# Optimization experiments

Hardware: AMD Instinct MI355X
Metric: run time of the kernel (lower is better)

The kernel has to match this reference:

```python
import jax, jax.numpy as jnp
import numpy as np

DIM = 512
HEADS = 8
HD = DIM // HEADS
HIDDEN = 4 * DIM
EPS = 1e-5


def layernorm(x, g, b):
    mu = jnp.mean(x, axis=-1, keepdims=True)
    var = jnp.mean(jnp.square(x - mu), axis=-1, keepdims=True)
    return (x - mu) * jax.lax.rsqrt(var + EPS) * g + b


def setup_inputs() -> dict:
    key = jax.random.key(0)
    ks = jax.random.split(key, 10)
    B, P, N, C = 16, 4, 256, DIM
    s = 1.0 / np.sqrt(C)
    sh = 1.0 / np.sqrt(HIDDEN)
    return {
        "x": jax.random.normal(ks[0], (B, P, N, C), jnp.float32),
        "ln1_g": jnp.ones((C,), jnp.float32),
        "ln1_b": jnp.zeros((C,), jnp.float32),
        "w_qkv": jax.random.uniform(ks[1], (3 * C, C), jnp.float32, -s, s),
        "w_proj": jax.random.uniform(ks[2], (C, C), jnp.float32, -s, s),
        "b_proj": jax.random.uniform(ks[3], (C,), jnp.float32, -s, s),
        "ln2_g": jnp.ones((C,), jnp.float32),
        "ln2_b": jnp.zeros((C,), jnp.float32),
        "w1": jax.random.uniform(ks[4], (HIDDEN, C), jnp.float32, -s, s),
        "b1": jax.random.uniform(ks[5], (HIDDEN,), jnp.float32, -s, s),
        "w2": jax.random.uniform(ks[6], (C, HIDDEN), jnp.float32, -sh, sh),
        "b2": jax.random.uniform(ks[7], (C,), jnp.float32, -sh, sh),
    }


def reference(x, ln1_g, ln1_b, w_qkv, w_proj, b_proj, ln2_g, ln2_b, w1, b1, w2, b2):
    B, P, N, C = x.shape
    # --- attention branch (batched over B, P, heads; same math as the unrolled loops) ---
    h = layernorm(x, ln1_g, ln1_b)
    qkv = jnp.einsum('bpnc,dc->bpnd', h, w_qkv)            # [B,P,N,3C]
    qkv = qkv.reshape(B, P, N, 3, HEADS, HD)
    q, k, v = qkv[..., 0, :, :], qkv[..., 1, :, :], qkv[..., 2, :, :]  # [B,P,N,H,hd]
    scale = HD ** -0.5
    attn = jnp.einsum('bpnhd,bpmhd->bphnm', q * scale, k)  # [B,P,H,N,N]
    attn = jax.nn.softmax(attn, axis=-1)
    o = jnp.einsum('bphnm,bpmhd->bpnhd', attn, v).reshape(B, P, N, C)
    o = jnp.einsum('bpnc,dc->bpnd', o, w_proj) + b_proj
    x = x + o
    # --- MLP branch ---
    h = layernorm(x, ln2_g, ln2_b)
    h = jax.nn.gelu(jnp.einsum('bpnc,hc->bpnh', h, w1) + b1, approximate=False)
    h = jnp.einsum('bpnh,ch->bpnc', h, w2) + b2
    return x + h
```

## Files before the change

kernel.cpp:

```cpp
#include <hip/hip_runtime.h>

typedef __attribute__((ext_vector_type(8))) short short8;
typedef __attribute__((ext_vector_type(4))) float f32x4;

__device__ __forceinline__ float bf2f(unsigned short u) {
    return __uint_as_float(((unsigned)u) << 16);
}
__device__ __forceinline__ unsigned short f2bf(float f) {
    unsigned u = __float_as_uint(f);
    u += 0x7fffu + ((u >> 16) & 1u);
    return (unsigned short)(u >> 16);
}
__device__ __forceinline__ void load_lds16(const void* g, void* l) {
    __builtin_amdgcn_global_load_lds(
        (const __attribute__((address_space(1))) void*)g,
        (__attribute__((address_space(3))) void*)l, 16, 0, 0);
}
__device__ __forceinline__ bool is_bf16(const unsigned* dt) {
    return *dt == 0x3F803F80u;
}
__device__ __forceinline__ float gelu_fast(float t) {
    float u = t * (0.7978845608f + 0.0356774081f * t * t);
    float e = __expf(-2.0f * fabsf(u));
    float th = (1.0f - e) / (1.0f + e);
    th = copysignf(th, u);
    return 0.5f * t * (1.0f + th);
}

__global__ __launch_bounds__(512) void cast_all(
    const void* s_wqkv, const void* s_wproj, const void* s_w1, const void* s_w2,
    const void* v0, const void* v1, const void* v2, const void* v3,
    const void* v4, const void* v5, const void* v6,
    unsigned short* d_wqkv, unsigned short* d_wproj, unsigned short* d_w1,
    unsigned short* d_w2, unsigned short* par, const unsigned* dt)
{
    bool isbf = is_bf16(dt);
    int b = blockIdx.x, tid = threadIdx.x;
    if (b < 768) {
        const void* src; unsigned short* dst; int off;
        if (b < 192)      { src = s_wqkv;  dst = d_wqkv;  off = b * 4096; }
        else if (b < 256) { src = s_wproj; dst = d_wproj; off = (b - 192) * 4096; }
        else if (b < 512) { src = s_w1;    dst = d_w1;    off = (b - 256) * 4096; }
        else              { src = s_w2;    dst = d_w2;    off = (b - 512) * 4096; }
        int i = off + tid * 8;
        if (isbf) {
            *(short8*)(dst + i) = *(const short8*)((const unsigned short*)src + i);
        } else {
            const float* s = (const float*)src + i;
            short8 o;
            #pragma unroll
            for (int j = 0; j < 8; ++j) o[j] = (short)f2bf(s[j]);
            *(short8*)(dst + i) = o;
        }
    } else {
        const void* srcs[7]  = {v0, v1, v2, v3, v4, v5, v6};
        const int   sizes[7] = {512, 512, 512, 512, 512, 2048, 512};
        const int   offs[7]  = {0, 512, 1024, 1536, 2048, 2560, 4608};
        int j = b - 768;
        const void* s = srcs[j];
        unsigned short* d = par + offs[j];
        for (int i = tid; i < sizes[j]; i += 512)
            d[i] = isbf ? ((const unsigned short*)s)[i] : f2bf(((const float*)s)[i]);
    }
}

__global__ __launch_bounds__(256) void ln_kernel(
    const void* __restrict__ xin, size_t row0,
    const unsigned* __restrict__ dt, int force_f32,
    const unsigned short* __restrict__ g, const unsigned short* __restrict__ b,
    unsigned short* __restrict__ y)
{
    int w = threadIdx.x >> 6, lane = threadIdx.x & 63;
    size_t lr = (size_t)blockIdx.x * 4 + w;
    size_t gr = row0 + lr;
    bool isf32 = force_f32 || !is_bf16(dt);
    float v[8];
    if (isf32) {
        const float* xr = (const float*)xin + (gr << 9) + (lane << 3);
        #pragma unroll
        for (int j = 0; j < 8; ++j) v[j] = xr[j];
    } else {
        short8 raw = *(const short8*)((const unsigned short*)xin + (gr << 9) + (lane << 3));
        #pragma unroll
        for (int j = 0; j < 8; ++j) v[j] = bf2f((unsigned short)raw[j]);
    }
    float sum = 0.f, sq = 0.f;
    #pragma unroll
    for (int j = 0; j < 8; ++j) { sum += v[j]; sq += v[j] * v[j]; }
    #pragma unroll
    for (int off = 32; off > 0; off >>= 1) {
        sum += __shfl_xor(sum, off);
        sq  += __shfl_xor(sq, off);
    }
    float mu  = sum * (1.0f / 512.0f);
    float var = sq * (1.0f / 512.0f) - mu * mu;
    float rs  = rsqrtf(var + 1e-5f);
    short8 gr8 = *(const short8*)(g + (lane << 3));
    short8 br8 = *(const short8*)(b + (lane << 3));
    short8 outv;
    #pragma unroll
    for (int j = 0; j < 8; ++j) {
        float o = (v[j] - mu) * rs * bf2f((unsigned short)gr8[j]) + bf2f((unsigned short)br8[j]);
        outv[j] = (short)f2bf(o);
    }
    *(short8*)(y + (lr << 9) + (lane << 3)) = outv;
}

__global__ __launch_bounds__(256, 2) void gemm5(
    const unsigned short* __restrict__ A, const unsigned short* __restrict__ W,
    const unsigned short* __restrict__ bias,
    const void* __restrict__ resid, size_t rrow0,
    void* __restrict__ out, size_t orow0,
    int NBY, int N, int K, int mode, const unsigned* __restrict__ dt)
{
    constexpr int BM = 256, BN = 128;
    constexpr int MI = 8;
    constexpr int BUFB = (BM + BN) * 64;
    __shared__ char lds[BM * BN * 2];

    int tid = threadIdx.x;
    int w = tid >> 6, lane = tid & 63;
    int l15 = lane & 15, g = lane >> 4;

    int L = blockIdx.x;
    int bx, by;
    if ((NBY & 7) == 0) {
        int nby8 = NBY >> 3;
        int xcd = L & 7, i = L >> 3;
        by = xcd * nby8 + (i % nby8);
        bx = i / nby8;
    } else {
        by = L % NBY;
        bx = L / NBY;
    }
    int m0 = by << 8, n0 = bx << 7;
    int wm = (w >> 1) << 7;
    int wn = (w & 1) << 6;

    int srow_t = ((tid >> 3) << 1) | (tid & 1);
    int u_t = ((tid >> 1) & 3) ^ ((tid >> 3) & 3);
    const unsigned short* gA[4];
    const unsigned short* gB[2];
    #pragma unroll
    for (int j = 0; j < 4; ++j)
        gA[j] = A + (size_t)(m0 + j * 64 + srow_t) * K + u_t * 8;
    #pragma unroll
    for (int j = 0; j < 2; ++j)
        gB[j] = W + (size_t)(n0 + j * 64 + srow_t) * K + u_t * 8;
    int lslot = tid * 16;

    int off = (l15 >> 1) * 128 + ((g ^ ((l15 >> 1) & 3)) << 5) + ((l15 & 1) << 4);

    f32x4 acc[MI][4];
    #pragma unroll
    for (int i = 0; i < MI; ++i)
        #pragma unroll
        for (int j = 0; j < 4; ++j) acc[i][j] = (f32x4){0.f, 0.f, 0.f, 0.f};

    #pragma unroll
    for (int j = 0; j < 4; ++j)
        load_lds16(gA[j], &lds[j * 4096 + lslot]);
    #pragma unroll
    for (int j = 0; j < 2; ++j)
        load_lds16(gB[j], &lds[16384 + j * 4096 + lslot]);

    int p = 0;
    for (int k = 0; k < K; k += 32) {
        __syncthreads();
        if (k + 32 < K) {
            int kn = k + 32;
            char* nb = &lds[(p ^ 1) * BUFB];
            #pragma unroll
            for (int j = 0; j < 4; ++j)
                load_lds16(gA[j] + kn, nb + j * 4096 + lslot);
            #pragma unroll
            for (int j = 0; j < 2; ++j)
                load_lds16(gB[j] + kn, nb + 16384 + j * 4096 + lslot);
        }
        const char* bA = &lds[p * BUFB];
        const char* bB = bA + 16384;
        short8 af[MI], bfr[4];
        #pragma unroll
        for (int i = 0; i < MI; ++i)
            af[i] = *(const short8*)(bA + (wm + i * 16) * 64 + off);
        #pragma unroll
        for (int j = 0; j < 4; ++j)
            bfr[j] = *(const short8*)(bB + (wn + j * 16) * 64 + off);
        #pragma unroll
        for (int i = 0; i < MI; ++i)
            #pragma unroll
            for (int j = 0; j < 4; ++j)
                acc[i][j] = __builtin_amdgcn_mfma_f32_16x16x32_bf16(af[i], bfr[j], acc[i][j], 0, 0, 0);
        p ^= 1;
    }

    char* tb = (char*)lds;
    __syncthreads();
    #pragma unroll
    for (int j = 0; j < 4; ++j) {
        int colL = wn + j * 16 + l15;
        int ccb = colL >> 3, cb = (colL & 7) << 1;
        #pragma unroll
        for (int i = 0; i < MI; ++i) {
            #pragma unroll
            for (int r = 0; r < 4; ++r) {
                int row = wm + i * 16 + g * 4 + r;
                *(unsigned short*)(tb + row * 256 + ((ccb ^ (row & 15)) << 4) + cb)
                    = f2bf(acc[i][j][r]);
            }
        }
    }
    __syncthreads();

    int rL = tid >> 4;
    int lc = tid & 15;
    bool inbf = is_bf16(dt);
    int colg = n0 + lc * 8;
    float bv[8];
    if (bias) {
        short8 bb = *(const short8*)(bias + colg);
        #pragma unroll
        for (int t = 0; t < 8; ++t) bv[t] = bf2f((unsigned short)bb[t]);
    } else {
        #pragma unroll
        for (int t = 0; t < 8; ++t) bv[t] = 0.f;
    }

    for (int ps = 0; ps < 16; ++ps) {
        int row = ps * 16 + rL;
        int rowL = m0 + row;
        short8 vv = *(const short8*)(tb + row * 256 + ((lc ^ (row & 15)) << 4));
        float vals[8];
        #pragma unroll
        for (int t = 0; t < 8; ++t) vals[t] = bf2f((unsigned short)vv[t]) + bv[t];

        if (mode == 0) {
            *(short8*)((unsigned short*)out + (size_t)rowL * N + colg) = vv;
        } else if (mode == 2) {
            short8 ov;
            #pragma unroll
            for (int t = 0; t < 8; ++t) ov[t] = (short)f2bf(gelu_fast(vals[t]));
            *(short8*)((unsigned short*)out + (size_t)rowL * N + colg) = ov;
        } else if (mode == 1) {
            size_t rbase = (rrow0 + rowL) * (size_t)N + colg;
            float o8[8];
            if (inbf) {
                short8 rr = *(const short8*)((const unsigned short*)resid + rbase);
                #pragma unroll
                for (int t = 0; t < 8; ++t) o8[t] = bf2f((unsigned short)rr[t]) + vals[t];
            } else {
                f32x4 r0 = *(const f32x4*)((const float*)resid + rbase);
                f32x4 r1 = *(const f32x4*)((const float*)resid + rbase + 4);
                #pragma unroll
                for (int t = 0; t < 4; ++t) { o8[t] = r0[t] + vals[t]; o8[t + 4] = r1[t] + vals[t + 4]; }
            }
            float* ob = (float*)out + (size_t)rowL * N + colg;
            *(f32x4*)ob       = (f32x4){o8[0], o8[1], o8[2], o8[3]};
            *(f32x4*)(ob + 4) = (f32x4){o8[4], o8[5], o8[6], o8[7]};
        } else {
            size_t rbase = (size_t)rowL * N + colg;
            f32x4 r0 = *(const f32x4*)((const float*)resid + rbase);
            f32x4 r1 = *(const f32x4*)((const float*)resid + rbase + 4);
            float o8[8];
            #pragma unroll
            for (int t = 0; t < 4; ++t) { o8[t] = r0[t] + vals[t]; o8[t + 4] = r1[t] + vals[t + 4]; }
            size_t obase = (orow0 + rowL) * (size_t)N + colg;
            if (inbf) {
                short8 ov;
                #pragma unroll
                for (int t = 0; t < 8; ++t) ov[t] = (short)f2bf(o8[t]);
                *(short8*)((unsigned short*)out + obase) = ov;
            } else {
                float* ob = (float*)out + obase;
                *(f32x4*)ob       = (f32x4){o8[0], o8[1], o8[2], o8[3]};
                *(f32x4*)(ob + 4) = (f32x4){o8[4], o8[5], o8[6], o8[7]};
            }
        }
    }
}

__global__ __launch_bounds__(256) void attn_mfma(
    const unsigned short* __restrict__ qkv, unsigned short* __restrict__ o)
{
    __shared__ unsigned short Vt[64 * 256];
    __shared__ unsigned short Ps[4][16 * 256];
    int bp = blockIdx.x >> 3, h = blockIdx.x & 7;
    const unsigned short* base = qkv + (size_t)bp * 256 * 1536;
    int qo = h << 6, ko = 512 + (h << 6), vo = 1024 + (h << 6);
    int tid = threadIdx.x, w = tid >> 6, lane = tid & 63;
    int l15 = lane & 15, g = lane >> 4;

    {
        int d = tid & 63;
        for (int s = tid >> 6; s < 256; s += 4) {
            unsigned short v = base[(size_t)s * 1536 + vo + d];
            *(unsigned short*)((char*)Vt + d * 512 + (((s >> 3) ^ (d & 7)) << 4) + ((s & 7) << 1)) = v;
        }
    }
    __syncthreads();

    unsigned short* P = Ps[w];

    for (int pass = 0; pass < 4; ++pass) {
        int q0 = pass * 64 + w * 16;
        short8 qa[2];
        #pragma unroll
        for (int t = 0; t < 2; ++t)
            qa[t] = *(const short8*)(base + (size_t)(q0 + l15) * 1536 + qo + t * 32 + g * 8);
        f32x4 S[16];
        #pragma unroll
        for (int ns = 0; ns < 16; ++ns) {
            f32x4 a = {0.f, 0.f, 0.f, 0.f};
            #pragma unroll
            for (int t = 0; t < 2; ++t) {
                short8 kb = *(const short8*)(base + (size_t)(ns * 16 + l15) * 1536 + ko + t * 32 + g * 8);
                a = __builtin_amdgcn_mfma_f32_16x16x32_bf16(qa[t], kb, a, 0, 0, 0);
            }
            S[ns] = a;
        }
        float mx[4], sums[4], inv[4];
        #pragma unroll
        for (int r = 0; r < 4; ++r) {
            float m = -1e30f;
            #pragma unroll
            for (int ns = 0; ns < 16; ++ns) m = fmaxf(m, S[ns][r]);
            m *= 0.125f;
            #pragma unroll
            for (int off = 1; off < 16; off <<= 1) m = fmaxf(m, __shfl_xor(m, off));
            mx[r] = m;
            sums[r] = 0.f;
        }
        #pragma unroll
        for (int ns = 0; ns < 16; ++ns)
            #pragma unroll
            for (int r = 0; r < 4; ++r) {
                float p = __expf(S[ns][r] * 0.125f - mx[r]);
                sums[r] += p;
                S[ns][r] = p;
            }
        #pragma unroll
        for (int r = 0; r < 4; ++r) {
            float s2 = sums[r];
            #pragma unroll
            for (int off = 1; off < 16; off <<= 1) s2 += __shfl_xor(s2, off);
            inv[r] = 1.0f / s2;
        }
        #pragma unroll
        for (int ns = 0; ns < 16; ++ns)
            #pragma unroll
            for (int r = 0; r < 4; ++r) {
                int mq = g * 4 + r;
                int s = ns * 16 + l15;
                *(unsigned short*)((char*)P + mq * 512 + (((s >> 3) ^ (mq & 7)) << 4) + ((s & 7) << 1))
                    = f2bf(S[ns][r] * inv[r]);
            }
        f32x4 O[4];
        #pragma unroll
        for (int ds = 0; ds < 4; ++ds) O[ds] = (f32x4){0.f, 0.f, 0.f, 0.f};
        #pragma unroll
        for (int ks = 0; ks < 8; ++ks) {
            int c = (ks * 4 + g) ^ (l15 & 7);
            short8 pa = *(const short8*)((const char*)P + l15 * 512 + (c << 4));
            #pragma unroll
            for (int ds = 0; ds < 4; ++ds) {
                short8 vb = *(const short8*)((const char*)Vt + (ds * 16 + l15) * 512 + (c << 4));
                O[ds] = __builtin_amdgcn_mfma_f32_16x16x32_bf16(pa, vb, O[ds], 0, 0, 0);
            }
        }
        #pragma unroll
        for (int ds = 0; ds < 4; ++ds)
            #pragma unroll
            for (int r = 0; r < 4; ++r) {
                int mq = q0 + g * 4 + r;
                int d = ds * 16 + l15;
                o[((size_t)(bp * 256 + mq) << 9) + (h << 6) + d] = f2bf(O[ds][r]);
            }
    }
}

extern "C" void kernel_launch(void* const* d_in, const int* in_sizes, int n_in,
                              void* d_out, int out_size, void* d_ws, size_t ws_size,
                              hipStream_t stream)
{
    const void* x      = d_in[0];
    const void* ln1_g  = d_in[1];
    const void* ln1_b  = d_in[2];
    const void* w_qkv  = d_in[3];
    const void* w_proj = d_in[4];
    const void* b_proj = d_in[5];
    const void* ln2_g  = d_in[6];
    const void* ln2_b  = d_in[7];
    const void* w1     = d_in[8];
    const void* b1     = d_in[9];
    const void* w2     = d_in[10];
    const void* b2     = d_in[11];
    const unsigned* dt = (const unsigned*)ln1_g;

    const int M = 16384;
    char* ws = (char*)d_ws;
    unsigned short* wqkv_b  = (unsigned short*)(ws);
    unsigned short* wproj_b = (unsigned short*)(ws + 1572864);
    unsigned short* w1_b    = (unsigned short*)(ws + 2097152);
    unsigned short* w2_b    = (unsigned short*)(ws + 4194304);
    unsigned short* par     = (unsigned short*)(ws + 6291456);
    const size_t CAST_END = 6308096;

    unsigned short* p_g1    = par + 0;
    unsigned short* p_b1ln  = par + 512;
    unsigned short* p_bproj = par + 1024;
    unsigned short* p_g2    = par + 1536;
    unsigned short* p_b2ln  = par + 2048;
    unsigned short* p_b1    = par + 2560;
    unsigned short* p_b2    = par + 4608;

    int NC = 64;
    const int cand[7] = {1, 2, 4, 8, 16, 32, 64};
    for (int i = 0; i < 7; ++i) {
        size_t need = CAST_END + (size_t)(M / cand[i]) * 11264;
        if (need <= ws_size) { NC = cand[i]; break; }
    }
    const int R = M / NC;
    const int NBY = R / 256;

    char* cb = ws + CAST_END;
    unsigned short* h   = (unsigned short*)(cb);
    unsigned short* qkv = (unsigned short*)(cb + (size_t)R * 1024);
    unsigned short* o   = (unsigned short*)(cb + (size_t)R * 4096);
    float*          x2  = (float*)        (cb + (size_t)R * 5120);
    unsigned short* hid = (unsigned short*)(cb + (size_t)R * 7168);
    unsigned short* h2  = h;

    cast_all<<<775, 512, 0, stream>>>(w_qkv, w_proj, w1, w2,
                                      ln1_g, ln1_b, b_proj, ln2_g, ln2_b, b1, b2,
                                      wqkv_b, wproj_b, w1_b, w2_b, par, dt);

    for (int c = 0; c < NC; ++c) {
        const size_t r0 = (size_t)c * R;

        ln_kernel<<<R / 4, 256, 0, stream>>>(x, r0, dt, 0, p_g1, p_b1ln, h);
        gemm5<<<(1536 / 128) * NBY, 256, 0, stream>>>(
            h, wqkv_b, nullptr, nullptr, 0, qkv, 0, NBY, 1536, 512, 0, dt);
        attn_mfma<<<(R / 256) * 8, 256, 0, stream>>>(qkv, o);
        gemm5<<<(512 / 128) * NBY, 256, 0, stream>>>(
            o, wproj_b, p_bproj, x, r0, x2, 0, NBY, 512, 512, 1, dt);
        ln_kernel<<<R / 4, 256, 0, stream>>>(x2, 0, dt, 1, p_g2, p_b2ln, h2);
        gemm5<<<(2048 / 128) * NBY, 256, 0, stream>>>(
            h2, w1_b, p_b1, nullptr, 0, hid, 0, NBY, 2048, 512, 2, dt);
        gemm5<<<(512 / 128) * NBY, 256, 0, stream>>>(
            hid, w2_b, p_b2, x2, 0, d_out, r0, NBY, 512, 2048, 3, dt);
    }
}
```

Before: 347.8 us.

## Template GEMM on row tile size, use smaller tiles for narrow-N GEMMs

The GEMM kernel becomes a template on BM, and the two N=512 GEMMs (projection and MLP down) use BM=128 with higher occupancy, launching twice as many blocks. The MFMA operand order is swapped so weights act as the A operand, and the epilogue writes packed 4-element bf16 pairs to LDS with a new swizzle instead of scalar 16-bit stores. This targets low block counts on the narrow GEMMs and slow scalar LDS stores in the epilogue. In exchange, the smaller tiles reload the weight tile for every row tile.

```diff
diff --git a/kernel.cpp b/kernel.cpp
--- a/kernel.cpp
+++ b/kernel.cpp
@@ -2,6 +2,7 @@
 
 typedef __attribute__((ext_vector_type(8))) short short8;
 typedef __attribute__((ext_vector_type(4))) float f32x4;
+typedef __attribute__((ext_vector_type(2))) unsigned int u32x2;
 
 __device__ __forceinline__ float bf2f(unsigned short u) {
     return __uint_as_float(((unsigned)u) << 16);
@@ -10,6 +11,9 @@
     unsigned u = __float_as_uint(f);
     u += 0x7fffu + ((u >> 16) & 1u);
     return (unsigned short)(u >> 16);
+}
+__device__ __forceinline__ unsigned pack2(float lo, float hi) {
+    return (unsigned)f2bf(lo) | ((unsigned)f2bf(hi) << 16);
 }
 __device__ __forceinline__ void load_lds16(const void* g, void* l) {
     __builtin_amdgcn_global_load_lds(
@@ -106,17 +110,20 @@
     *(short8*)(y + (lr << 9) + (lane << 3)) = outv;
 }
 
-__global__ __launch_bounds__(256, 2) void gemm5(
+template<int BM>
+__global__ __launch_bounds__(256, (BM == 128) ? 4 : 2) void gemm6(
     const unsigned short* __restrict__ A, const unsigned short* __restrict__ W,
     const unsigned short* __restrict__ bias,
     const void* __restrict__ resid, size_t rrow0,
     void* __restrict__ out, size_t orow0,
     int NBY, int N, int K, int mode, const unsigned* __restrict__ dt)
 {
-    constexpr int BM = 256, BN = 128;
-    constexpr int MI = 8;
+    constexpr int BN = 128;
+    constexpr int MJ = BM / 32;
+    constexpr int AR = BM / 64;
     constexpr int BUFB = (BM + BN) * 64;
-    __shared__ char lds[BM * BN * 2];
+    constexpr int LDSZ = (2 * BUFB > BM * BN * 2) ? 2 * BUFB : BM * BN * 2;
+    __shared__ char lds[LDSZ];
 
     int tid = threadIdx.x;
     int w = tid >> 6, lane = tid & 63;
@@ -133,16 +140,16 @@
         by = L % NBY;
         bx = L / NBY;
     }
-    int m0 = by << 8, n0 = bx << 7;
-    int wm = (w >> 1) << 7;
+    int m0 = by * BM, n0 = bx * BN;
+    int wm = (BM == 256) ? ((w >> 1) << 7) : ((w >> 1) << 6);
     int wn = (w & 1) << 6;
 
     int srow_t = ((tid >> 3) << 1) | (tid & 1);
     int u_t = ((tid >> 1) & 3) ^ ((tid >> 3) & 3);
-    const unsigned short* gA[4];
+    const unsigned short* gA[AR];
     const unsigned short* gB[2];
     #pragma unroll
-    for (int j = 0; j < 4; ++j)
+    for (int j = 0; j < AR; ++j)
         gA[j] = A + (size_t)(m0 + j * 64 + srow_t) * K + u_t * 8;
     #pragma unroll
     for (int j = 0; j < 2; ++j)
@@ -151,18 +158,18 @@
 
     int off = (l15 >> 1) * 128 + ((g ^ ((l15 >> 1) & 3)) << 5) + ((l15 & 1) << 4);
 
-    f32x4 acc[MI][4];
-    #pragma unroll
-    for (int i = 0; i < MI; ++i)
-        #pragma unroll
-        for (int j = 0; j < 4; ++j) acc[i][j] = (f32x4){0.f, 0.f, 0.f, 0.f};
-
-    #pragma unroll
-    for (int j = 0; j < 4; ++j)
+    f32x4 acc[4][MJ];
+    #pragma unroll
+    for (int i = 0; i < 4; ++i)
+        #pragma unroll
+        for (int j = 0; j < MJ; ++j) acc[i][j] = (f32x4){0.f, 0.f, 0.f, 0.f};
+
+    #pragma unroll
+    for (int j = 0; j < AR; ++j)
         load_lds16(gA[j], &lds[j * 4096 + lslot]);
     #pragma unroll
     for (int j = 0; j < 2; ++j)
-        load_lds16(gB[j], &lds[16384 + j * 4096 + lslot]);
+        load_lds16(gB[j], &lds[BM * 64 + j * 4096 + lslot]);
 
     int p = 0;
     for (int k = 0; k < K; k += 32) {
@@ -171,43 +178,42 @@
             int kn = k + 32;
             char* nb = &lds[(p ^ 1) * BUFB];
             #pragma unroll
-            for (int j = 0; j < 4; ++j)
+            for (int j = 0; j < AR; ++j)
                 load_lds16(gA[j] + kn, nb + j * 4096 + lslot);
             #pragma unroll
             for (int j = 0; j < 2; ++j)
-                load_lds16(gB[j] + kn, nb + 16384 + j * 4096 + lslot);
-        }
-        const char* bA = &lds[p * BUFB];
-        const char* bB = bA + 16384;
-        short8 af[MI], bfr[4];
-        #pragma unroll
-        for (int i = 0; i < MI; ++i)
-            af[i] = *(const short8*)(bA + (wm + i * 16) * 64 + off);
-        #pragma unroll
-        for (int j = 0; j < 4; ++j)
-            bfr[j] = *(const short8*)(bB + (wn + j * 16) * 64 + off);
-        #pragma unroll
-        for (int i = 0; i < MI; ++i)
-            #pragma unroll
-            for (int j = 0; j < 4; ++j)
-                acc[i][j] = __builtin_amdgcn_mfma_f32_16x16x32_bf16(af[i], bfr[j], acc[i][j], 0, 0, 0);
+                load_lds16(gB[j] + kn, nb + BM * 64 + j * 4096 + lslot);
+        }
+        const char* bAct = &lds[p * BUFB];
+        const char* bW = bAct + BM * 64;
+        short8 wf[4], af[MJ];
+        #pragma unroll
+        for (int i = 0; i < 4; ++i)
+            wf[i] = *(const short8*)(bW + (wn + i * 16) * 64 + off);
+        #pragma unroll
+        for (int j = 0; j < MJ; ++j)
+            af[j] = *(const short8*)(bAct + (wm + j * 16) * 64 + off);
+        #pragma unroll
+        for (int i = 0; i < 4; ++i)
+            #pragma unroll
+            for (int j = 0; j < MJ; ++j)
+                acc[i][j] = __builtin_amdgcn_mfma_f32_16x16x32_bf16(wf[i], af[j], acc[i][j], 0, 0, 0);
         p ^= 1;
     }
 
     char* tb = (char*)lds;
     __syncthreads();
     #pragma unroll
-    for (int j = 0; j < 4; ++j) {
-        int colL = wn + j * 16 + l15;
-        int ccb = colL >> 3, cb = (colL & 7) << 1;
-        #pragma unroll
-        for (int i = 0; i < MI; ++i) {
-            #pragma unroll
-            for (int r = 0; r < 4; ++r) {
-                int row = wm + i * 16 + g * 4 + r;
-                *(unsigned short*)(tb + row * 256 + ((ccb ^ (row & 15)) << 4) + cb)
-                    = f2bf(acc[i][j][r]);
-            }
+    for (int j = 0; j < MJ; ++j) {
+        int mloc = wm + j * 16 + l15;
+        char* rowp = tb + mloc * (BN * 2);
+        int sw = mloc & (BN / 4 - 2);
+        #pragma unroll
+        for (int i = 0; i < 4; ++i) {
+            int cq = (wn + i * 16 + g * 4) >> 2;
+            u32x2 pk = {pack2(acc[i][j][0], acc[i][j][1]),
+                        pack2(acc[i][j][2], acc[i][j][3])};
+            *(u32x2*)(rowp + ((cq ^ sw) << 3)) = pk;
         }
     }
     __syncthreads();
@@ -226,10 +232,12 @@
         for (int t = 0; t < 8; ++t) bv[t] = 0.f;
     }
 
-    for (int ps = 0; ps < 16; ++ps) {
+    #pragma unroll 4
+    for (int ps = 0; ps < BM / 16; ++ps) {
         int row = ps * 16 + rL;
         int rowL = m0 + row;
-        short8 vv = *(const short8*)(tb + row * 256 + ((lc ^ (row & 15)) << 4));
+        int c16 = lc ^ ((row >> 1) & 15);
+        short8 vv = *(const short8*)(tb + row * (BN * 2) + (c16 << 4));
         float vals[8];
         #pragma unroll
         for (int t = 0; t < 8; ++t) vals[t] = bf2f((unsigned short)vv[t]) + bv[t];
@@ -420,7 +428,6 @@
         if (need <= ws_size) { NC = cand[i]; break; }
     }
     const int R = M / NC;
-    const int NBY = R / 256;
 
     char* cb = ws + CAST_END;
     unsigned short* h   = (unsigned short*)(cb);
@@ -438,15 +445,15 @@
         const size_t r0 = (size_t)c * R;
 
         ln_kernel<<<R / 4, 256, 0, stream>>>(x, r0, dt, 0, p_g1, p_b1ln, h);
-        gemm5<<<(1536 / 128) * NBY, 256, 0, stream>>>(
-            h, wqkv_b, nullptr, nullptr, 0, qkv, 0, NBY, 1536, 512, 0, dt);
+        gemm6<256><<<(1536 / 128) * (R / 256), 256, 0, stream>>>(
+            h, wqkv_b, nullptr, nullptr, 0, qkv, 0, R / 256, 1536, 512, 0, dt);
         attn_mfma<<<(R / 256) * 8, 256, 0, stream>>>(qkv, o);
-        gemm5<<<(512 / 128) * NBY, 256, 0, stream>>>(
-            o, wproj_b, p_bproj, x, r0, x2, 0, NBY, 512, 512, 1, dt);
+        gemm6<128><<<(512 / 128) * (R / 128), 256, 0, stream>>>(
+            o, wproj_b, p_bproj, x, r0, x2, 0, R / 128, 512, 512, 1, dt);
         ln_kernel<<<R / 4, 256, 0, stream>>>(x2, 0, dt, 1, p_g2, p_b2ln, h2);
-        gemm5<<<(2048 / 128) * NBY, 256, 0, stream>>>(
-            h2, w1_b, p_b1, nullptr, 0, hid, 0, NBY, 2048, 512, 2, dt);
-        gemm5<<<(512 / 128) * NBY, 256, 0, stream>>>(
-            hid, w2_b, p_b2, x2, 0, d_out, r0, NBY, 512, 2048, 3, dt);
-    }
-}
+        gemm6<256><<<(2048 / 128) * (R / 256), 256, 0, stream>>>(
+            h2, w1_b, p_b1, nullptr, 0, hid, 0, R / 256, 2048, 512, 2, dt);
+        gemm6<128><<<(512 / 128) * (R / 128), 256, 0, stream>>>(
+            hid, w2_b, p_b2, x2, 0, d_out, r0, R / 128, 512, 2048, 3, dt);
+    }
+}
```

New measurement: 336.4 us. -3.3%, faster.
